# Optimization experiments

Hardware: AMD Instinct MI355X
Metric: run time of the kernel (lower is better)

The kernel has to match this reference:

```python
import jax, jax.numpy as jnp
import numpy as np

B, T, D_IN, H, D_OUT = 64, 256, 512, 1024, 512
SCALE0 = 1.0 / np.float32(np.sqrt(D_IN + H))   # layer 0: sqrt(input+hidden)
SCALE1 = 1.0 / np.float32(np.sqrt(H + H))      # layer 1: sqrt(hidden+hidden)


def setup_inputs() -> dict:
    key = jax.random.key(0)
    ks = jax.random.split(key, 7)
    s0 = 1.0 / np.sqrt(D_IN + H)
    s1 = 1.0 / np.sqrt(H + H)
    return {
        "x": jax.random.normal(ks[0], (B, T, D_IN), dtype=jnp.float32),
        # fused gate weights, gate order along last axis: [f, i, o, c]
        "W0": jax.random.normal(ks[1], (D_IN + H, 4 * H), dtype=jnp.float32) * s0,
        "b0": jax.random.normal(ks[2], (4 * H,), dtype=jnp.float32) * 0.01,
        "W1": jax.random.normal(ks[3], (H + H, 4 * H), dtype=jnp.float32) * s1,
        "b1": jax.random.normal(ks[4], (4 * H,), dtype=jnp.float32) * 0.01,
        "Wfc": jax.random.normal(ks[5], (H, D_OUT), dtype=jnp.float32) * (1.0 / np.sqrt(H)),
        "bfc": jax.random.normal(ks[6], (D_OUT,), dtype=jnp.float32) * 0.01,
    }


def _cell(inp, h, c, W, b, scale):
    # fused 4-gate GEMM: [B, in+H] @ [in+H, 4H]
    z = (jnp.concatenate([inp, h], axis=1) @ W + b) * scale
    f, i, o, g = jnp.split(z, 4, axis=1)
    f = jax.nn.sigmoid(f)
    i = jax.nn.sigmoid(i)
    o = jax.nn.sigmoid(o)
    g = jnp.tanh(g)
    c_t = f * c + i * g
    h_t = o * jnp.tanh(c_t)
    return h_t, c_t


def reference(x, W0, b0, W1, b1, Wfc, bfc):
    Bx = x.shape[0]
    h0 = jnp.zeros((Bx, H), x.dtype)
    c0 = jnp.zeros((Bx, H), x.dtype)
    h1 = jnp.zeros((Bx, H), x.dtype)
    c1 = jnp.zeros((Bx, H), x.dtype)

    def step(carry, xt):
        h0, c0, h1, c1 = carry
        h0, c0 = _cell(xt, h0, c0, W0, b0, SCALE0)
        h1, c1 = _cell(h0, h1, c1, W1, b1, SCALE1)
        return (h0, c0, h1, c1), None

    xs = jnp.swapaxes(x, 0, 1)  # [T, B, D_IN]
    (h0, c0, h1, c1), _ = jax.lax.scan(step, (h0, c0, h1, c1), xs)
    return h1 @ Wfc + bfc
```

## Files before the change

kernel.cpp:

```cpp
#include <hip/hip_runtime.h>
#include <hip/hip_bf16.h>

typedef __attribute__((ext_vector_type(8))) short bf16x8;
typedef __attribute__((ext_vector_type(4))) float f32x4;
using bf16 = __hip_bfloat16;
typedef unsigned long long u64;

constexpr int BB = 64, TT = 256, DIN = 512, HH = 1024, DOUT = 512;
constexpr int P0 = 1544;
constexpr int P1 = 2056;
constexpr int HWORDS = 8192;
constexpr int NW = 8;

#define MFMA16(a, b, c) __builtin_amdgcn_mfma_f32_16x16x32_bf16((a), (b), (c), 0, 0, 0)
#define ALOAD(p)  __hip_atomic_load((p),  __ATOMIC_RELAXED, __HIP_MEMORY_SCOPE_AGENT)
#define ASTORE(p, v) __hip_atomic_store((p), (v), __ATOMIC_RELAXED, __HIP_MEMORY_SCOPE_AGENT)

union frag_u { u64 q[2]; bf16x8 f; };

__device__ __forceinline__ short f2b(float f) {
  __hip_bfloat16 h = __float2bfloat16(f);
  return *reinterpret_cast<short*>(&h);
}
__device__ __forceinline__ u64 pack4(float4 v) {
  return (u64)(unsigned short)f2b(v.x) | ((u64)(unsigned short)f2b(v.y) << 16) |
         ((u64)(unsigned short)f2b(v.z) << 32) | ((u64)(unsigned short)f2b(v.w) << 48);
}

__device__ __forceinline__ unsigned short gates(const float zv[4], const float br[4],
                                                float scale, float& cr, bool first) {
  float zf = (zv[0] + br[0]) * scale;
  float zi = (zv[1] + br[1]) * scale;
  float zo = (zv[2] + br[2]) * scale;
  float zg = (zv[3] + br[3]) * scale;
  float f = 1.0f / (1.0f + __expf(-zf));
  float i = 1.0f / (1.0f + __expf(-zi));
  float o = 1.0f / (1.0f + __expf(-zo));
  float g = tanhf(zg);
  float cn = f * (first ? 0.0f : cr) + i * g;
  cr = cn;
  __hip_bfloat16 hv = __float2bfloat16(o * tanhf(cn));
  return *reinterpret_cast<unsigned short*>(&hv);
}

__global__ void __launch_bounds__(512, 1)
lstm_persist(const float* __restrict__ x,  const float* __restrict__ W0,
             const float* __restrict__ b0, const float* __restrict__ W1,
             const float* __restrict__ b1, const float* __restrict__ Wfc,
             const float* __restrict__ bfc,
             u64* __restrict__ xbu, int use_xb,
             u64* __restrict__ h0s, u64* __restrict__ h1s,
             unsigned* __restrict__ flagsA, unsigned* __restrict__ flagsB,
             float* __restrict__ out) {
  __shared__ unsigned short lw0[16 * P0];
  __shared__ unsigned short lw1[16 * P1];
  __shared__ float zbuf[NW][4][16][17];
  __shared__ unsigned short hs[64][4];

  const int tid  = threadIdx.x;
  const int wg   = blockIdx.x;
  const int lane = tid & 63;
  const int wv   = tid >> 6;
  const int n    = lane & 15;
  const int oct  = lane >> 4;
  const int mg   = tid & 63;
  const int hq   = tid >> 6;
  const float S0 = 1.0f / sqrtf((float)(DIN + HH));
  const float S1 = 1.0f / sqrtf((float)(HH + HH));

  float c0r = 0.0f, c1r = 0.0f;
  float b0r[4] = {0, 0, 0, 0}, b1r[4] = {0, 0, 0, 0};
  if (tid < 256) {
    const int hcol = wg * 4 + hq;
#pragma unroll
    for (int g = 0; g < 4; ++g) { b0r[g] = b0[g * HH + hcol]; b1r[g] = b1[g * HH + hcol]; }
  }

  {
    const int g = tid >> 7, kw = tid & 127;
    const int col0 = g * HH + wg * 4;
    for (int k = kw; k < DIN + HH; k += 128) {
      float4 u = *(const float4*)(W0 + (size_t)k * 4096 + col0);
      lw0[(g * 4 + 0) * P0 + k] = (unsigned short)f2b(u.x);
      lw0[(g * 4 + 1) * P0 + k] = (unsigned short)f2b(u.y);
      lw0[(g * 4 + 2) * P0 + k] = (unsigned short)f2b(u.z);
      lw0[(g * 4 + 3) * P0 + k] = (unsigned short)f2b(u.w);
    }
    for (int k = kw; k < 2 * HH; k += 128) {
      float4 u = *(const float4*)(W1 + (size_t)k * 4096 + col0);
      lw1[(g * 4 + 0) * P1 + k] = (unsigned short)f2b(u.x);
      lw1[(g * 4 + 1) * P1 + k] = (unsigned short)f2b(u.y);
      lw1[(g * 4 + 2) * P1 + k] = (unsigned short)f2b(u.z);
      lw1[(g * 4 + 3) * P1 + k] = (unsigned short)f2b(u.w);
    }
  }

  if (use_xb) {
    const int t = wg;
    for (int u = tid; u < 64 * 64; u += 512) {
      const int row = u & 63, ko = u >> 6;
      const float* p = x + ((size_t)row * TT + t) * DIN + ko * 8;
      float4 A = *(const float4*)p, B = *(const float4*)(p + 4);
      u64* d = xbu + ((size_t)(t * 64 + ko) * 64 + row) * 2;
      ASTORE(d, pack4(A));
      ASTORE(d + 1, pack4(B));
    }
  }
  __syncthreads();

  f32x4 z0a[4], z1a[4];
  float zv[4] = {0, 0, 0, 0};

  auto flag_release = [&](unsigned* f, unsigned val) {
    if (tid < 64) __builtin_amdgcn_s_waitcnt(0);
    if (tid == 0) ASTORE(f + wg, val);
  };
  auto bar_wait = [&](unsigned* f, unsigned target) {
    if (tid < 64) {
      const u64* p = (const u64*)(f + tid * 4);
      for (;;) {
        u64 a = ALOAD(p), b = ALOAD(p + 1);
        if ((unsigned)a >= target && (unsigned)(a >> 32) >= target &&
            (unsigned)b >= target && (unsigned)(b >> 32) >= target) break;
        __builtin_amdgcn_s_sleep(1);
      }
    }
    __syncthreads();
    __builtin_amdgcn_fence(__ATOMIC_ACQUIRE, "workgroup");
  };

  flag_release(flagsA, 1u);
  bar_wait(flagsA, 1u);

  auto xpart = [&](int t) {
    if (use_xb) {
      const bf16* xb = (const bf16*)xbu;
#pragma unroll
      for (int s = 0; s < 2; ++s) {
        const int ko = wv * 8 + s * 4 + oct;
        bf16x8 bw = *(const bf16x8*)&lw0[n * P0 + ko * 8];
#pragma unroll
        for (int rt = 0; rt < 4; ++rt) {
          bf16x8 a = *(const bf16x8*)(xb + ((size_t)(t * 64 + ko) * 64 + rt * 16 + n) * 8);
          z0a[rt] = MFMA16(a, bw, z0a[rt]);
        }
      }
    } else {
#pragma unroll
      for (int s = 0; s < 2; ++s) {
        const int kp = wv * 64 + s * 32 + oct * 8;
        bf16x8 bw = *(const bf16x8*)&lw0[n * P0 + kp];
#pragma unroll
        for (int rt = 0; rt < 4; ++rt) {
          const float* p = x + ((size_t)(rt * 16 + n) * TT + t) * DIN + kp;
          float4 A = *(const float4*)p, B = *(const float4*)(p + 4);
          bf16x8 a;
          a[0] = f2b(A.x); a[1] = f2b(A.y); a[2] = f2b(A.z); a[3] = f2b(A.w);
          a[4] = f2b(B.x); a[5] = f2b(B.y); a[6] = f2b(B.z); a[7] = f2b(B.w);
          z0a[rt] = MFMA16(a, bw, z0a[rt]);
        }
      }
    }
  };

  auto h0gemm = [&](const u64* h0b) {
    u64 lo[16], hi[16];
#pragma unroll
    for (int i = 0; i < 16; ++i) {
      const int s = i >> 2, rt = i & 3;
      const int idx = (wv * 16 + s * 4 + oct) * 64 + rt * 16 + n;
      lo[i] = ALOAD(h0b + idx);
      hi[i] = ALOAD(h0b + HWORDS + idx);
    }
#pragma unroll
    for (int s = 0; s < 4; ++s) {
      const int kp = wv * 128 + s * 32 + oct * 8;
      bf16x8 bw0 = *(const bf16x8*)&lw0[n * P0 + 512 + kp];
      bf16x8 bw1 = *(const bf16x8*)&lw1[n * P1 + kp];
#pragma unroll
      for (int rt = 0; rt < 4; ++rt) {
        frag_u u; u.q[0] = lo[s * 4 + rt]; u.q[1] = hi[s * 4 + rt];
        z0a[rt] = MFMA16(u.f, bw0, z0a[rt]);
        z1a[rt] = MFMA16(u.f, bw1, z1a[rt]);
      }
    }
  };
  auto h1gemm = [&](const u64* hb, int koff) {
    u64 lo[16], hi[16];
#pragma unroll
    for (int i = 0; i < 16; ++i) {
      const int s = i >> 2, rt = i & 3;
      const int idx = (wv * 16 + s * 4 + oct) * 64 + rt * 16 + n;
      lo[i] = ALOAD(hb + idx);
      hi[i] = ALOAD(hb + HWORDS + idx);
    }
#pragma unroll
    for (int s = 0; s < 4; ++s) {
      const int kp = wv * 128 + s * 32 + oct * 8;
      bf16x8 bw = *(const bf16x8*)&lw1[n * P1 + koff + kp];
#pragma unroll
      for (int rt = 0; rt < 4; ++rt) {
        frag_u u; u.q[0] = lo[s * 4 + rt]; u.q[1] = hi[s * 4 + rt];
        z1a[rt] = MFMA16(u.f, bw, z1a[rt]);
      }
    }
  };

  auto publish = [&](u64* dst) {
    if (tid < 64) {
      u64 val = *(const u64*)&hs[tid][0];
      ASTORE(dst + (size_t)(wg & 1) * HWORDS + (wg >> 1) * 64 + tid, val);
    }
  };
  auto zreduce = [&](f32x4 za[4]) {
#pragma unroll
    for (int rt = 0; rt < 4; ++rt)
#pragma unroll
      for (int r = 0; r < 4; ++r) zbuf[wv][rt][oct * 4 + r][n] = za[rt][r];
    __syncthreads();
    if (tid < 256) {
#pragma unroll
      for (int g = 0; g < 4; ++g) {
        float s = 0.f;
#pragma unroll
        for (int w = 0; w < NW; ++w) s += zbuf[w][mg >> 4][mg & 15][g * 4 + hq];
        zv[g] = s;
      }
    }
  };

#pragma unroll
  for (int rt = 0; rt < 4; ++rt) z0a[rt] = (f32x4){0.f, 0.f, 0.f, 0.f};
  xpart(0);
  zreduce(z0a);
  if (tid < 256) hs[mg][hq] = gates(zv, b0r, S0, c0r, true);
  __syncthreads();
  publish(h0s);
  flag_release(flagsA, 2u);
  flag_release(flagsB, 1u);
#pragma unroll
  for (int rt = 0; rt < 4; ++rt) z0a[rt] = (f32x4){0.f, 0.f, 0.f, 0.f};
  xpart(1);

  for (int t = 1; t < TT; ++t) {
    bar_wait(flagsA, (unsigned)t + 1u);
    const u64* h0b = h0s + (size_t)(((t - 1) & 1) * 2) * HWORDS;
#pragma unroll
    for (int rt = 0; rt < 4; ++rt) z1a[rt] = (f32x4){0.f, 0.f, 0.f, 0.f};
    h0gemm(h0b);

    zreduce(z0a);
    if (tid < 256) hs[mg][hq] = gates(zv, b0r, S0, c0r, false);
    __syncthreads();
    publish(h0s + (size_t)((t & 1) * 2) * HWORDS);
    flag_release(flagsA, (unsigned)t + 2u);

    if (t < TT - 1) {
#pragma unroll
      for (int rt = 0; rt < 4; ++rt) z0a[rt] = (f32x4){0.f, 0.f, 0.f, 0.f};
      xpart(t + 1);
    }

    if (t >= 2) {
      bar_wait(flagsB, (unsigned)t);
      h1gemm(h1s + (size_t)((t & 1) * 2) * HWORDS, 1024);
    }
    zreduce(z1a);
    if (tid < 256) hs[mg][hq] = gates(zv, b1r, S1, c1r, t == 1);
    __syncthreads();
    publish(h1s + (size_t)(((t - 1) & 1) * 2) * HWORDS);
    flag_release(flagsB, (unsigned)t + 1u);
  }

  {
    bar_wait(flagsA, 257u);
#pragma unroll
    for (int rt = 0; rt < 4; ++rt) z1a[rt] = (f32x4){0.f, 0.f, 0.f, 0.f};
    h1gemm(h0s + 2 * HWORDS, 0);
    bar_wait(flagsB, 256u);
    h1gemm(h1s, 1024);
    zreduce(z1a);
    if (tid < 256) hs[mg][hq] = gates(zv, b1r, S1, c1r, false);
    __syncthreads();
    publish(h1s + 2 * HWORDS);
    flag_release(flagsB, 257u);
  }

  if (wg < DOUT / 16) {
    bar_wait(flagsB, 257u);
    {
      const int q = tid >> 7, kw = tid & 127;
      for (int k = kw; k < HH; k += 128) {
        float4 u = *(const float4*)(Wfc + (size_t)k * DOUT + wg * 16 + q * 4);
        lw0[(q * 4 + 0) * P0 + k] = (unsigned short)f2b(u.x);
        lw0[(q * 4 + 1) * P0 + k] = (unsigned short)f2b(u.y);
        lw0[(q * 4 + 2) * P0 + k] = (unsigned short)f2b(u.z);
        lw0[(q * 4 + 3) * P0 + k] = (unsigned short)f2b(u.w);
      }
    }
    __syncthreads();
    if (tid < 256) {
      const int v4 = tid >> 6;
      const u64* hb = h1s + 2 * HWORDS;
      f32x4 acc0 = {0.f, 0.f, 0.f, 0.f}, acc1 = {0.f, 0.f, 0.f, 0.f};
#pragma unroll
      for (int it = 0; it < 16; ++it) {
        const int idxA = (it * 8 + oct) * 64 + v4 * 16 + n;
        const int idxB = (it * 8 + 4 + oct) * 64 + v4 * 16 + n;
        frag_u uA, uB;
        uA.q[0] = ALOAD(hb + idxA); uA.q[1] = ALOAD(hb + HWORDS + idxA);
        uB.q[0] = ALOAD(hb + idxB); uB.q[1] = ALOAD(hb + HWORDS + idxB);
        bf16x8 bwA = *(const bf16x8*)&lw0[n * P0 + it * 64 + oct * 8];
        bf16x8 bwB = *(const bf16x8*)&lw0[n * P0 + it * 64 + 32 + oct * 8];
        acc0 = MFMA16(uA.f, bwA, acc0);
        acc1 = MFMA16(uB.f, bwB, acc1);
      }
      float bb = bfc[wg * 16 + n];
#pragma unroll
      for (int r = 0; r < 4; ++r) {
        int row = v4 * 16 + oct * 4 + r;
        out[(size_t)row * DOUT + wg * 16 + n] = acc0[r] + acc1[r] + bb;
      }
    }
  }
}

extern "C" void kernel_launch(void* const* d_in, const int* in_sizes, int n_in,
                              void* d_out, int out_size, void* d_ws, size_t ws_size,
                              hipStream_t stream) {
  const float* x   = (const float*)d_in[0];
  const float* W0  = (const float*)d_in[1];
  const float* b0  = (const float*)d_in[2];
  const float* W1  = (const float*)d_in[3];
  const float* b1  = (const float*)d_in[4];
  const float* Wfc = (const float*)d_in[5];
  const float* bfc = (const float*)d_in[6];

  char* ws = (char*)d_ws;
  unsigned* flagsA = (unsigned*)ws;
  unsigned* flagsB = (unsigned*)(ws + 1024);
  u64* h0s = (u64*)(ws + 4096);
  u64* h1s = h0s + 4 * HWORDS;
  u64* xbu = h1s + 4 * HWORDS;
  size_t needed = 4096 + 2 * 4 * (size_t)HWORDS * 8 + (size_t)TT * 64 * 64 * 16;
  int use_xb = (ws_size >= needed) ? 1 : 0;

  hipMemsetAsync(ws, 0, 4096, stream);

  lstm_persist<<<dim3(256), dim3(512), 0, stream>>>(
      x, W0, b0, W1, b1, Wfc, bfc, xbu, use_xb, h0s, h1s, flagsA, flagsB, (float*)d_out);
}
```

Measured before the change: 2.243 ms.

## Interleave hidden-state halves and prefetch h1 loads before x-part MFMAs

The published hidden-state buffers change layout so that the lo and hi 8-byte halves of each unit sit next to each other (16 contiguous bytes) rather than in two planes HWORDS apart, which makes the two atomic loads per fragment adjacent. The layer-1 recurrent h loads are also issued right after the flagsB barrier and before the x-part MFMAs for the next step, so their global latency overlaps with that compute. The cost is 32 extra live u64 registers across xpart, which could raise register pressure and lower occupancy, and layer-1 now waits on flagsB before running xpart.

```diff
diff --git a/kernel.cpp b/kernel.cpp
--- a/kernel.cpp
+++ b/kernel.cpp
@@ -9,7 +9,8 @@
 constexpr int BB = 64, TT = 256, DIN = 512, HH = 1024, DOUT = 512;
 constexpr int P0 = 1544;
 constexpr int P1 = 2056;
-constexpr int HWORDS = 8192;
+constexpr int HUNITS = 8192;
+constexpr int PARSTRIDE = 2 * HUNITS;
 constexpr int NW = 8;
 
 #define MFMA16(a, b, c) __builtin_amdgcn_mfma_f32_16x16x32_bf16((a), (b), (c), 0, 0, 0)
@@ -128,6 +129,9 @@
     __syncthreads();
     __builtin_amdgcn_fence(__ATOMIC_ACQUIRE, "workgroup");
   };
+  auto hslot = [&](u64* arr, int t) -> u64* {
+    return arr + (size_t)(t & 1) * PARSTRIDE;
+  };
 
   flag_release(flagsA, 1u);
   bar_wait(flagsA, 1u);
@@ -163,15 +167,19 @@
     }
   };
 
-  auto h0gemm = [&](const u64* h0b) {
-    u64 lo[16], hi[16];
+  auto hload = [&](const u64* hb, u64 lo[16], u64 hi[16]) {
 #pragma unroll
     for (int i = 0; i < 16; ++i) {
       const int s = i >> 2, rt = i & 3;
       const int idx = (wv * 16 + s * 4 + oct) * 64 + rt * 16 + n;
-      lo[i] = ALOAD(h0b + idx);
-      hi[i] = ALOAD(h0b + HWORDS + idx);
-    }
+      lo[i] = ALOAD(hb + 2 * idx);
+      hi[i] = ALOAD(hb + 2 * idx + 1);
+    }
+  };
+
+  auto h0gemm = [&](const u64* h0b) {
+    u64 lo[16], hi[16];
+    hload(h0b, lo, hi);
 #pragma unroll
     for (int s = 0; s < 4; ++s) {
       const int kp = wv * 128 + s * 32 + oct * 8;
@@ -185,15 +193,7 @@
       }
     }
   };
-  auto h1gemm = [&](const u64* hb, int koff) {
-    u64 lo[16], hi[16];
-#pragma unroll
-    for (int i = 0; i < 16; ++i) {
-      const int s = i >> 2, rt = i & 3;
-      const int idx = (wv * 16 + s * 4 + oct) * 64 + rt * 16 + n;
-      lo[i] = ALOAD(hb + idx);
-      hi[i] = ALOAD(hb + HWORDS + idx);
-    }
+  auto h1mfma = [&](const u64 lo[16], const u64 hi[16], int koff) {
 #pragma unroll
     for (int s = 0; s < 4; ++s) {
       const int kp = wv * 128 + s * 32 + oct * 8;
@@ -209,7 +209,8 @@
   auto publish = [&](u64* dst) {
     if (tid < 64) {
       u64 val = *(const u64*)&hs[tid][0];
-      ASTORE(dst + (size_t)(wg & 1) * HWORDS + (wg >> 1) * 64 + tid, val);
+      const size_t unit = (size_t)(wg >> 1) * 64 + tid;
+      ASTORE(dst + unit * 2 + (wg & 1), val);
     }
   };
   auto zreduce = [&](f32x4 za[4]) {
@@ -235,7 +236,7 @@
   zreduce(z0a);
   if (tid < 256) hs[mg][hq] = gates(zv, b0r, S0, c0r, true);
   __syncthreads();
-  publish(h0s);
+  publish(hslot(h0s, 0));
   flag_release(flagsA, 2u);
   flag_release(flagsB, 1u);
 #pragma unroll
@@ -244,31 +245,32 @@
 
   for (int t = 1; t < TT; ++t) {
     bar_wait(flagsA, (unsigned)t + 1u);
-    const u64* h0b = h0s + (size_t)(((t - 1) & 1) * 2) * HWORDS;
 #pragma unroll
     for (int rt = 0; rt < 4; ++rt) z1a[rt] = (f32x4){0.f, 0.f, 0.f, 0.f};
-    h0gemm(h0b);
+    h0gemm(hslot(h0s, t - 1));
 
     zreduce(z0a);
     if (tid < 256) hs[mg][hq] = gates(zv, b0r, S0, c0r, false);
     __syncthreads();
-    publish(h0s + (size_t)((t & 1) * 2) * HWORDS);
+    publish(hslot(h0s, t));
     flag_release(flagsA, (unsigned)t + 2u);
 
+    u64 lo1[16], hi1[16];
+    if (t >= 2) {
+      bar_wait(flagsB, (unsigned)t);
+      hload(hslot(h1s, t - 2), lo1, hi1);
+    }
     if (t < TT - 1) {
 #pragma unroll
       for (int rt = 0; rt < 4; ++rt) z0a[rt] = (f32x4){0.f, 0.f, 0.f, 0.f};
       xpart(t + 1);
     }
-
-    if (t >= 2) {
-      bar_wait(flagsB, (unsigned)t);
-      h1gemm(h1s + (size_t)((t & 1) * 2) * HWORDS, 1024);
-    }
+    if (t >= 2) h1mfma(lo1, hi1, 1024);
+
     zreduce(z1a);
     if (tid < 256) hs[mg][hq] = gates(zv, b1r, S1, c1r, t == 1);
     __syncthreads();
-    publish(h1s + (size_t)(((t - 1) & 1) * 2) * HWORDS);
+    publish(hslot(h1s, t - 1));
     flag_release(flagsB, (unsigned)t + 1u);
   }
 
@@ -276,13 +278,21 @@
     bar_wait(flagsA, 257u);
 #pragma unroll
     for (int rt = 0; rt < 4; ++rt) z1a[rt] = (f32x4){0.f, 0.f, 0.f, 0.f};
-    h1gemm(h0s + 2 * HWORDS, 0);
+    {
+      u64 lo1[16], hi1[16];
+      hload(hslot(h0s, 255), lo1, hi1);
+      h1mfma(lo1, hi1, 0);
+    }
     bar_wait(flagsB, 256u);
-    h1gemm(h1s, 1024);
+    {
+      u64 lo1[16], hi1[16];
+      hload(hslot(h1s, 254), lo1, hi1);
+      h1mfma(lo1, hi1, 1024);
+    }
     zreduce(z1a);
     if (tid < 256) hs[mg][hq] = gates(zv, b1r, S1, c1r, false);
     __syncthreads();
-    publish(h1s + 2 * HWORDS);
+    publish(hslot(h1s, 255));
     flag_release(flagsB, 257u);
   }
 
@@ -301,15 +311,15 @@
     __syncthreads();
     if (tid < 256) {
       const int v4 = tid >> 6;
-      const u64* hb = h1s + 2 * HWORDS;
+      const u64* hb = hslot(h1s, 255);
       f32x4 acc0 = {0.f, 0.f, 0.f, 0.f}, acc1 = {0.f, 0.f, 0.f, 0.f};
 #pragma unroll
       for (int it = 0; it < 16; ++it) {
         const int idxA = (it * 8 + oct) * 64 + v4 * 16 + n;
         const int idxB = (it * 8 + 4 + oct) * 64 + v4 * 16 + n;
         frag_u uA, uB;
-        uA.q[0] = ALOAD(hb + idxA); uA.q[1] = ALOAD(hb + HWORDS + idxA);
-        uB.q[0] = ALOAD(hb + idxB); uB.q[1] = ALOAD(hb + HWORDS + idxB);
+        uA.q[0] = ALOAD(hb + 2 * idxA); uA.q[1] = ALOAD(hb + 2 * idxA + 1);
+        uB.q[0] = ALOAD(hb + 2 * idxB); uB.q[1] = ALOAD(hb + 2 * idxB + 1);
         bf16x8 bwA = *(const bf16x8*)&lw0[n * P0 + it * 64 + oct * 8];
         bf16x8 bwB = *(const bf16x8*)&lw0[n * P0 + it * 64 + 32 + oct * 8];
         acc0 = MFMA16(uA.f, bwA, acc0);
@@ -340,9 +350,9 @@
   unsigned* flagsA = (unsigned*)ws;
   unsigned* flagsB = (unsigned*)(ws + 1024);
   u64* h0s = (u64*)(ws + 4096);
-  u64* h1s = h0s + 4 * HWORDS;
-  u64* xbu = h1s + 4 * HWORDS;
-  size_t needed = 4096 + 2 * 4 * (size_t)HWORDS * 8 + (size_t)TT * 64 * 64 * 16;
+  u64* h1s = h0s + 2 * (size_t)PARSTRIDE;
+  u64* xbu = h1s + 2 * (size_t)PARSTRIDE;
+  size_t needed = 4096 + 4 * (size_t)PARSTRIDE * 8 + (size_t)TT * 64 * 64 * 16;
   int use_xb = (ws_size >= needed) ? 1 : 0;
 
   hipMemsetAsync(ws, 0, 4096, stream);
```

New measurement: 2.504 ms. 11.7% more time.
